# Performance work log

Hardware: AMD Instinct MI355X
Metric: run time of the kernel (lower is better)

## Reference

```python
import jax, jax.numpy as jnp
import numpy as np
import math

N, D, H = 4096, 2048, 16
HD = D // H  # head_dim = 128


def setup_inputs() -> dict:
    key = jax.random.key(0)
    ks = jax.random.split(key, 9)
    s = 1.0 / math.sqrt(D)
    return {
        "x":  jax.random.normal(ks[0], (N, D), dtype=jnp.float32),
        "Wq": jax.random.normal(ks[1], (D, D), dtype=jnp.float32) * s,
        "bq": jax.random.normal(ks[2], (D,), dtype=jnp.float32) * s,
        "Wk": jax.random.normal(ks[3], (D, D), dtype=jnp.float32) * s,
        "bk": jax.random.normal(ks[4], (D,), dtype=jnp.float32) * s,
        "Wv": jax.random.normal(ks[5], (D, D), dtype=jnp.float32) * s,
        "bv": jax.random.normal(ks[6], (D,), dtype=jnp.float32) * s,
        "Wo": jax.random.normal(ks[7], (D, D), dtype=jnp.float32) * s,
        "bo": jax.random.normal(ks[8], (D,), dtype=jnp.float32) * s,
    }


def reference(x, Wq, bq, Wk, bk, Wv, bv, Wo, bo):
    # eqx.nn.Linear: y = W @ x + b, weight shape (out, in) -> x @ W.T + b
    q = x @ Wq.T + bq            # [N, D]
    k = x @ Wk.T + bk            # [N, D]
    v = x @ Wv.T + bv            # [N, D]
    q = q.reshape(N, H, HD).transpose(1, 0, 2)   # [H, N, hd]
    k = k.reshape(N, H, HD).transpose(1, 2, 0)   # [H, hd, N]
    v = v.reshape(N, H, HD).transpose(1, 0, 2)   # [H, N, hd]
    scale = 1.0 / math.sqrt(HD)
    scores = jnp.matmul(q * scale, k)            # [H, N, N]
    attn = jax.nn.softmax(scores, axis=-1)
    ctx = jnp.matmul(attn, v)                    # [H, N, hd]
    ctx = ctx.transpose(1, 0, 2).reshape(N, D)   # [N, D]
    return ctx @ Wo.T + bo
```

## Files before the change

### kernel.cpp

```cpp
#include <hip/hip_runtime.h>
#include <stdint.h>

#define N_TOK 4096
#define DIM   2048
#define NH    16
#define HD    128
#define NW    (DIM * DIM)

using bf16x8 = __attribute__((ext_vector_type(8))) short;
using bf16x4 = __attribute__((ext_vector_type(4))) short;
using f32x4  = __attribute__((ext_vector_type(4))) float;

#if __has_builtin(__builtin_amdgcn_exp2f)
#define EXP2(x) __builtin_amdgcn_exp2f(x)
#else
#define EXP2(x) exp2f(x)
#endif

__device__ inline unsigned short f2bf(float f) {
  union { float f; unsigned u; } v; v.f = f;
  unsigned r = v.u + 0x7FFFu + ((v.u >> 16) & 1u);
  return (unsigned short)(r >> 16);
}
__device__ inline float bf2f(unsigned short u) {
  union { unsigned u; float f; } v; v.u = ((unsigned)u) << 16; return v.f;
}
__device__ inline f32x4 mfma16(bf16x8 a, bf16x8 b, f32x4 c) {
  return __builtin_amdgcn_mfma_f32_16x16x32_bf16(a, b, c, 0, 0, 0);
}
__device__ inline void gll16(const unsigned short* g, unsigned short* l) {
  __builtin_amdgcn_global_load_lds(
      (const __attribute__((address_space(1))) void*)g,
      (__attribute__((address_space(3))) void*)l, 16, 0, 0);
}

__global__ __launch_bounds__(256)
void cvt_bf16(const float* __restrict__ src, unsigned short* __restrict__ dst, int n) {
  int i = blockIdx.x * 256 + threadIdx.x;
  if (i * 8 >= n) return;
  const float4* s = (const float4*)src + (size_t)i * 2;
  float4 a = s[0], b = s[1];
  bf16x8 o;
  o[0] = (short)f2bf(a.x); o[1] = (short)f2bf(a.y);
  o[2] = (short)f2bf(a.z); o[3] = (short)f2bf(a.w);
  o[4] = (short)f2bf(b.x); o[5] = (short)f2bf(b.y);
  o[6] = (short)f2bf(b.z); o[7] = (short)f2bf(b.w);
  *(bf16x8*)(dst + (size_t)i * 8) = o;
}

template<int OUT_MODE>
__global__ __launch_bounds__(256)
void gemm_bf16(const unsigned short* __restrict__ A, const unsigned short* __restrict__ B,
               const float* __restrict__ bias, void* __restrict__ out_, float scale) {
  __shared__ unsigned short Asl[128 * 32];
  __shared__ unsigned short Bsl[128 * 32];
  const int tid  = threadIdx.x;
  const int lane = tid & 63, w = tid >> 6;
  const int wy = w >> 1, wx = w & 1;
  const int lr = lane & 15, quad = lane >> 4;
  const int m0 = blockIdx.y * 128, n0 = blockIdx.x * 128;

  const f32x4 vzero = {0.f, 0.f, 0.f, 0.f};
  f32x4 acc[4][4];
#pragma unroll
  for (int i = 0; i < 4; ++i)
#pragma unroll
    for (int j = 0; j < 4; ++j) acc[i][j] = vzero;

  for (int k0 = 0; k0 < DIM; k0 += 32) {
    __syncthreads();
#pragma unroll
    for (int i = 0; i < 2; ++i) {
      int ch = tid + i * 256;
      int r = ch >> 2, cc = ch & 3;
      gll16(&A[(size_t)(m0 + r) * DIM + k0 + cc * 8], &Asl[ch * 8]);
      gll16(&B[(size_t)(n0 + r) * DIM + k0 + cc * 8], &Bsl[ch * 8]);
    }
    __syncthreads();

    bf16x8 af[4], bfv[4];
#pragma unroll
    for (int mb = 0; mb < 4; ++mb)
      af[mb] = *(const bf16x8*)&Asl[(wy * 64 + mb * 16 + lr) * 32 + quad * 8];
#pragma unroll
    for (int nb = 0; nb < 4; ++nb)
      bfv[nb] = *(const bf16x8*)&Bsl[(wx * 64 + nb * 16 + lr) * 32 + quad * 8];
#pragma unroll
    for (int mb = 0; mb < 4; ++mb)
#pragma unroll
      for (int nb = 0; nb < 4; ++nb)
        acc[mb][nb] = mfma16(af[mb], bfv[nb], acc[mb][nb]);
  }

#pragma unroll
  for (int mb = 0; mb < 4; ++mb)
#pragma unroll
    for (int nb = 0; nb < 4; ++nb) {
      int gn = n0 + wx * 64 + nb * 16 + lr;
      int gm_base = m0 + wy * 64 + mb * 16 + quad * 4;
      float bs = bias[gn];
      if constexpr (OUT_MODE == 2) {
        bf16x4 pk;
#pragma unroll
        for (int r = 0; r < 4; ++r) pk[r] = (short)f2bf((acc[mb][nb][r] + bs) * scale);
        *(bf16x4*)&((unsigned short*)out_)[(size_t)gn * N_TOK + gm_base] = pk;
      } else {
#pragma unroll
        for (int r = 0; r < 4; ++r) {
          float v = (acc[mb][nb][r] + bs) * scale;
          if constexpr (OUT_MODE == 1)
            ((float*)out_)[(size_t)(gm_base + r) * DIM + gn] = v;
          else
            ((unsigned short*)out_)[(size_t)(gm_base + r) * DIM + gn] = f2bf(v);
        }
      }
    }
}

__global__ __launch_bounds__(256)
void flash_attn(const unsigned short* __restrict__ Q,
                const unsigned short* __restrict__ K,
                const unsigned short* __restrict__ Vt,
                unsigned short* __restrict__ ctx) {
  constexpr int LDK = 136;
  constexpr int LDV = 72;
  constexpr int LDP = 72;
  __shared__ unsigned short Ksl[64 * LDK];
  __shared__ unsigned short VTsl[128 * LDV];
  __shared__ unsigned short Psl[4][32 * LDP];

  const int tid  = threadIdx.x;
  const int lane = tid & 63, w = tid >> 6;
  const int lr = lane & 15, quad = lane >> 4;
  const int hoff = blockIdx.y * HD;
  const int q0   = blockIdx.x * 128;
  const int qw   = q0 + w * 32;

  bf16x8 qf[2][4];
#pragma unroll
  for (int mb = 0; mb < 2; ++mb)
#pragma unroll
    for (int c = 0; c < 4; ++c)
      qf[mb][c] = *(const bf16x8*)&Q[(size_t)(qw + mb * 16 + lr) * DIM + hoff + c * 32 + quad * 8];

  const f32x4 vzero = {0.f, 0.f, 0.f, 0.f};
  f32x4 o[2][8];
  float l_part[2][4];
#pragma unroll
  for (int mb = 0; mb < 2; ++mb) {
#pragma unroll
    for (int nb = 0; nb < 8; ++nb) o[mb][nb] = vzero;
#pragma unroll
    for (int r = 0; r < 4; ++r) l_part[mb][r] = 0.f;
  }

  bf16x8 kreg[4], vreg[4];
  auto load_tile = [&](int kt) {
    int kbase = kt * 64;
#pragma unroll
    for (int i = 0; i < 4; ++i) {
      int ch = tid + i * 256;
      kreg[i] = *(const bf16x8*)&K[(size_t)(kbase + (ch >> 4)) * DIM + hoff + (ch & 15) * 8];
      vreg[i] = *(const bf16x8*)&Vt[(size_t)(hoff + (ch >> 3)) * N_TOK + kbase + (ch & 7) * 8];
    }
  };
  load_tile(0);

  for (int kt = 0; kt < N_TOK / 64; ++kt) {
    __syncthreads();
#pragma unroll
    for (int i = 0; i < 4; ++i) {
      int ch = tid + i * 256;
      *(bf16x8*)&Ksl[(ch >> 4) * LDK + (ch & 15) * 8] = kreg[i];
      *(bf16x8*)&VTsl[(ch >> 3) * LDV + (ch & 7) * 8] = vreg[i];
    }
    __syncthreads();
    if (kt + 1 < N_TOK / 64) load_tile(kt + 1);

    f32x4 s[2][4];
#pragma unroll
    for (int mb = 0; mb < 2; ++mb)
#pragma unroll
      for (int nf = 0; nf < 4; ++nf) s[mb][nf] = vzero;
#pragma unroll
    for (int nf = 0; nf < 4; ++nf)
#pragma unroll
      for (int c = 0; c < 4; ++c) {
        bf16x8 kf = *(const bf16x8*)&Ksl[(nf * 16 + lr) * LDK + c * 32 + quad * 8];
#pragma unroll
        for (int mb = 0; mb < 2; ++mb) s[mb][nf] = mfma16(qf[mb][c], kf, s[mb][nf]);
      }

#pragma unroll
    for (int mb = 0; mb < 2; ++mb)
#pragma unroll
      for (int nf = 0; nf < 4; ++nf)
#pragma unroll
        for (int r = 0; r < 4; ++r) {
          unsigned short us = f2bf(EXP2(s[mb][nf][r]));
          l_part[mb][r] += bf2f(us);
          Psl[w][(mb * 16 + quad * 4 + r) * LDP + nf * 16 + lr] = us;
        }
    __asm__ volatile("s_waitcnt lgkmcnt(0)" ::: "memory");

    bf16x8 pf[2][2];
#pragma unroll
    for (int mb = 0; mb < 2; ++mb)
#pragma unroll
      for (int ki = 0; ki < 2; ++ki)
        pf[mb][ki] = *(const bf16x8*)&Psl[w][(mb * 16 + lr) * LDP + ki * 32 + quad * 8];

#pragma unroll
    for (int nb = 0; nb < 8; ++nb)
#pragma unroll
      for (int ki = 0; ki < 2; ++ki) {
        bf16x8 vf = *(const bf16x8*)&VTsl[(nb * 16 + lr) * LDV + ki * 32 + quad * 8];
#pragma unroll
        for (int mb = 0; mb < 2; ++mb) o[mb][nb] = mfma16(pf[mb][ki], vf, o[mb][nb]);
      }
  }

#pragma unroll
  for (int mb = 0; mb < 2; ++mb)
#pragma unroll
    for (int r = 0; r < 4; ++r) {
      float t = l_part[mb][r];
      t += __shfl_xor(t, 1);
      t += __shfl_xor(t, 2);
      t += __shfl_xor(t, 4);
      t += __shfl_xor(t, 8);
      float inv = 1.0f / t;
      int gq = qw + mb * 16 + quad * 4 + r;
#pragma unroll
      for (int nb = 0; nb < 8; ++nb)
        ctx[(size_t)gq * DIM + hoff + nb * 16 + lr] = f2bf(o[mb][nb][r] * inv);
    }
}

extern "C" void kernel_launch(void* const* d_in, const int* in_sizes, int n_in,
                              void* d_out, int out_size, void* d_ws, size_t ws_size,
                              hipStream_t stream) {
  (void)in_sizes; (void)n_in; (void)out_size; (void)ws_size;
  const float* x  = (const float*)d_in[0];
  const float* Wq = (const float*)d_in[1];
  const float* bq = (const float*)d_in[2];
  const float* Wk = (const float*)d_in[3];
  const float* bk = (const float*)d_in[4];
  const float* Wv = (const float*)d_in[5];
  const float* bv = (const float*)d_in[6];
  const float* Wo = (const float*)d_in[7];
  const float* bo = (const float*)d_in[8];

  const size_t NE = (size_t)N_TOK * DIM;
  unsigned short* xb  = (unsigned short*)d_ws;
  unsigned short* Wqb = xb + NE;
  unsigned short* Wkb = Wqb + NW;
  unsigned short* Wvb = Wkb + NW;
  unsigned short* Wob = Wvb + NW;
  unsigned short* Qb  = Wob + NW;
  unsigned short* Kb  = Qb + NE;
  unsigned short* Vtb = Kb + NE;

  cvt_bf16<<<4096, 256, 0, stream>>>(x,  xb,  (int)NE);
  cvt_bf16<<<2048, 256, 0, stream>>>(Wq, Wqb, NW);
  cvt_bf16<<<2048, 256, 0, stream>>>(Wk, Wkb, NW);
  cvt_bf16<<<2048, 256, 0, stream>>>(Wv, Wvb, NW);
  cvt_bf16<<<2048, 256, 0, stream>>>(Wo, Wob, NW);

  dim3 gemm_grid(DIM / 128, N_TOK / 128);
  const float qscale = 1.4426950408889634f * 0.08838834764831845f;

  gemm_bf16<0><<<gemm_grid, 256, 0, stream>>>(xb, Wqb, bq, Qb, qscale);
  gemm_bf16<0><<<gemm_grid, 256, 0, stream>>>(xb, Wkb, bk, Kb, 1.0f);
  gemm_bf16<2><<<gemm_grid, 256, 0, stream>>>(xb, Wvb, bv, Vtb, 1.0f);

  unsigned short* ctxb = xb;
  flash_attn<<<dim3(N_TOK / 128, NH), 256, 0, stream>>>(Qb, Kb, Vtb, ctxb);

  gemm_bf16<1><<<gemm_grid, 256, 0, stream>>>(ctxb, Wob, bo, (float*)d_out, 1.0f);
}
```

Measured before the change: 531.6 us.

## Merge conversion and QKV launches, shrink attention tile and reuse K LDS for P

Folds the five fp32-to-bf16 conversion launches into one kernel, and merges the three Q/K/V projection GEMMs into one launch with a 48-wide grid. Flash attention now gives each wave 16 query rows instead of 32, and 64 query rows per block. It packs P into bf16 pairs through lane shuffles and stores them in the K shared-memory region, with an extra barrier before doing so. The row sum now accumulates unrounded fp32 exp values. The aim is to cut launch overhead, raise occupancy (launch bounds 256,4, smaller LDS) and reduce LDS traffic, at the cost of reading K/V twice as often per query and one more sync per tile.

```diff
diff --git a/kernel.cpp b/kernel.cpp
--- a/kernel.cpp
+++ b/kernel.cpp
@@ -22,8 +22,9 @@
   unsigned r = v.u + 0x7FFFu + ((v.u >> 16) & 1u);
   return (unsigned short)(r >> 16);
 }
-__device__ inline float bf2f(unsigned short u) {
-  union { unsigned u; float f; } v; v.u = ((unsigned)u) << 16; return v.f;
+__device__ inline unsigned pack_bf16(float lo, float hi) {
+  union { float f; unsigned u; } a, b; a.f = lo; b.f = hi;
+  return ((b.u + 0x8000u) & 0xFFFF0000u) | ((a.u + 0x8000u) >> 16);
 }
 __device__ inline f32x4 mfma16(bf16x8 a, bf16x8 b, f32x4 c) {
   return __builtin_amdgcn_mfma_f32_16x16x32_bf16(a, b, c, 0, 0, 0);
@@ -35,23 +36,107 @@
 }
 
 __global__ __launch_bounds__(256)
-void cvt_bf16(const float* __restrict__ src, unsigned short* __restrict__ dst, int n) {
-  int i = blockIdx.x * 256 + threadIdx.x;
-  if (i * 8 >= n) return;
-  const float4* s = (const float4*)src + (size_t)i * 2;
-  float4 a = s[0], b = s[1];
+void cvt_all(const float* __restrict__ x, const float* __restrict__ wq,
+             const float* __restrict__ wk, const float* __restrict__ wv,
+             const float* __restrict__ wo,
+             unsigned short* __restrict__ xb, unsigned short* __restrict__ wqb,
+             unsigned short* __restrict__ wkb, unsigned short* __restrict__ wvb,
+             unsigned short* __restrict__ wob) {
+  int bid = blockIdx.x;
+  const float* s; unsigned short* d; int lb;
+  if (bid < 4096) { s = x; d = xb; lb = bid; }
+  else {
+    int t = (bid - 4096) >> 11, r = (bid - 4096) & 2047;
+    s = (t == 0) ? wq : (t == 1) ? wk : (t == 2) ? wv : wo;
+    d = (t == 0) ? wqb : (t == 1) ? wkb : (t == 2) ? wvb : wob;
+    lb = r;
+  }
+  size_t i = ((size_t)lb * 256 + threadIdx.x) * 8;
+  const float4* sp = (const float4*)(s + i);
+  float4 a = sp[0], b = sp[1];
   bf16x8 o;
   o[0] = (short)f2bf(a.x); o[1] = (short)f2bf(a.y);
   o[2] = (short)f2bf(a.z); o[3] = (short)f2bf(a.w);
   o[4] = (short)f2bf(b.x); o[5] = (short)f2bf(b.y);
   o[6] = (short)f2bf(b.z); o[7] = (short)f2bf(b.w);
-  *(bf16x8*)(dst + (size_t)i * 8) = o;
-}
-
-template<int OUT_MODE>
+  *(bf16x8*)(d + i) = o;
+}
+
 __global__ __launch_bounds__(256)
-void gemm_bf16(const unsigned short* __restrict__ A, const unsigned short* __restrict__ B,
-               const float* __restrict__ bias, void* __restrict__ out_, float scale) {
+void gemm_qkv(const unsigned short* __restrict__ A,
+              const unsigned short* __restrict__ Bq, const unsigned short* __restrict__ Bk,
+              const unsigned short* __restrict__ Bv,
+              const float* __restrict__ bq, const float* __restrict__ bk,
+              const float* __restrict__ bv,
+              unsigned short* __restrict__ Qb, unsigned short* __restrict__ Kb,
+              unsigned short* __restrict__ Vtb, float qscale) {
+  __shared__ unsigned short Asl[128 * 32];
+  __shared__ unsigned short Bsl[128 * 32];
+  const int wsel = blockIdx.x >> 4;
+  const unsigned short* B = (wsel == 0) ? Bq : (wsel == 1) ? Bk : Bv;
+  const float* bias = (wsel == 0) ? bq : (wsel == 1) ? bk : bv;
+  const float scale = (wsel == 0) ? qscale : 1.0f;
+  const int tid  = threadIdx.x;
+  const int lane = tid & 63, w = tid >> 6;
+  const int wy = w >> 1, wx = w & 1;
+  const int lr = lane & 15, quad = lane >> 4;
+  const int m0 = blockIdx.y * 128, n0 = (blockIdx.x & 15) * 128;
+
+  const f32x4 vzero = {0.f, 0.f, 0.f, 0.f};
+  f32x4 acc[4][4];
+#pragma unroll
+  for (int i = 0; i < 4; ++i)
+#pragma unroll
+    for (int j = 0; j < 4; ++j) acc[i][j] = vzero;
+
+  for (int k0 = 0; k0 < DIM; k0 += 32) {
+    __syncthreads();
+#pragma unroll
+    for (int i = 0; i < 2; ++i) {
+      int ch = tid + i * 256;
+      int r = ch >> 2, cc = ch & 3;
+      gll16(&A[(size_t)(m0 + r) * DIM + k0 + cc * 8], &Asl[ch * 8]);
+      gll16(&B[(size_t)(n0 + r) * DIM + k0 + cc * 8], &Bsl[ch * 8]);
+    }
+    __syncthreads();
+    bf16x8 af[4], bfv[4];
+#pragma unroll
+    for (int mb = 0; mb < 4; ++mb)
+      af[mb] = *(const bf16x8*)&Asl[(wy * 64 + mb * 16 + lr) * 32 + quad * 8];
+#pragma unroll
+    for (int nb = 0; nb < 4; ++nb)
+      bfv[nb] = *(const bf16x8*)&Bsl[(wx * 64 + nb * 16 + lr) * 32 + quad * 8];
+#pragma unroll
+    for (int mb = 0; mb < 4; ++mb)
+#pragma unroll
+      for (int nb = 0; nb < 4; ++nb)
+        acc[mb][nb] = mfma16(af[mb], bfv[nb], acc[mb][nb]);
+  }
+
+#pragma unroll
+  for (int mb = 0; mb < 4; ++mb)
+#pragma unroll
+    for (int nb = 0; nb < 4; ++nb) {
+      int gn = n0 + wx * 64 + nb * 16 + lr;
+      int gm_base = m0 + wy * 64 + mb * 16 + quad * 4;
+      float bs = bias[gn];
+      if (wsel == 2) {
+        bf16x4 pk;
+#pragma unroll
+        for (int r = 0; r < 4; ++r) pk[r] = (short)f2bf(acc[mb][nb][r] + bs);
+        *(bf16x4*)&Vtb[(size_t)gn * N_TOK + gm_base] = pk;
+      } else {
+        unsigned short* out = (wsel == 0) ? Qb : Kb;
+#pragma unroll
+        for (int r = 0; r < 4; ++r)
+          out[(size_t)(gm_base + r) * DIM + gn] = f2bf((acc[mb][nb][r] + bs) * scale);
+      }
+    }
+}
+
+__global__ __launch_bounds__(256)
+void gemm_out(const unsigned short* __restrict__ A, const unsigned short* __restrict__ B,
+              const float* __restrict__ bias, float* __restrict__ out) {
   __shared__ unsigned short Asl[128 * 32];
   __shared__ unsigned short Bsl[128 * 32];
   const int tid  = threadIdx.x;
@@ -77,7 +162,6 @@
       gll16(&B[(size_t)(n0 + r) * DIM + k0 + cc * 8], &Bsl[ch * 8]);
     }
     __syncthreads();
-
     bf16x8 af[4], bfv[4];
 #pragma unroll
     for (int mb = 0; mb < 4; ++mb)
@@ -99,60 +183,41 @@
       int gn = n0 + wx * 64 + nb * 16 + lr;
       int gm_base = m0 + wy * 64 + mb * 16 + quad * 4;
       float bs = bias[gn];
-      if constexpr (OUT_MODE == 2) {
-        bf16x4 pk;
-#pragma unroll
-        for (int r = 0; r < 4; ++r) pk[r] = (short)f2bf((acc[mb][nb][r] + bs) * scale);
-        *(bf16x4*)&((unsigned short*)out_)[(size_t)gn * N_TOK + gm_base] = pk;
-      } else {
-#pragma unroll
-        for (int r = 0; r < 4; ++r) {
-          float v = (acc[mb][nb][r] + bs) * scale;
-          if constexpr (OUT_MODE == 1)
-            ((float*)out_)[(size_t)(gm_base + r) * DIM + gn] = v;
-          else
-            ((unsigned short*)out_)[(size_t)(gm_base + r) * DIM + gn] = f2bf(v);
-        }
-      }
-    }
-}
-
-__global__ __launch_bounds__(256)
+#pragma unroll
+      for (int r = 0; r < 4; ++r)
+        out[(size_t)(gm_base + r) * DIM + gn] = acc[mb][nb][r] + bs;
+    }
+}
+
+__global__ __launch_bounds__(256, 4)
 void flash_attn(const unsigned short* __restrict__ Q,
                 const unsigned short* __restrict__ K,
                 const unsigned short* __restrict__ Vt,
                 unsigned short* __restrict__ ctx) {
-  constexpr int LDK = 136;
+  constexpr int LDK = 144;
   constexpr int LDV = 72;
   constexpr int LDP = 72;
   __shared__ unsigned short Ksl[64 * LDK];
   __shared__ unsigned short VTsl[128 * LDV];
-  __shared__ unsigned short Psl[4][32 * LDP];
 
   const int tid  = threadIdx.x;
   const int lane = tid & 63, w = tid >> 6;
   const int lr = lane & 15, quad = lane >> 4;
   const int hoff = blockIdx.y * HD;
-  const int q0   = blockIdx.x * 128;
-  const int qw   = q0 + w * 32;
-
-  bf16x8 qf[2][4];
-#pragma unroll
-  for (int mb = 0; mb < 2; ++mb)
-#pragma unroll
-    for (int c = 0; c < 4; ++c)
-      qf[mb][c] = *(const bf16x8*)&Q[(size_t)(qw + mb * 16 + lr) * DIM + hoff + c * 32 + quad * 8];
+  const int qw   = blockIdx.x * 64 + w * 16;
+  const bool odd = lane & 1;
+  unsigned short* Pw = Ksl + w * (16 * LDP);
+
+  bf16x8 qf[4];
+#pragma unroll
+  for (int c = 0; c < 4; ++c)
+    qf[c] = *(const bf16x8*)&Q[(size_t)(qw + lr) * DIM + hoff + c * 32 + quad * 8];
 
   const f32x4 vzero = {0.f, 0.f, 0.f, 0.f};
-  f32x4 o[2][8];
-  float l_part[2][4];
-#pragma unroll
-  for (int mb = 0; mb < 2; ++mb) {
-#pragma unroll
-    for (int nb = 0; nb < 8; ++nb) o[mb][nb] = vzero;
-#pragma unroll
-    for (int r = 0; r < 4; ++r) l_part[mb][r] = 0.f;
-  }
+  f32x4 o[8];
+  float l_part[4] = {0.f, 0.f, 0.f, 0.f};
+#pragma unroll
+  for (int nb = 0; nb < 8; ++nb) o[nb] = vzero;
 
   bf16x8 kreg[4], vreg[4];
   auto load_tile = [&](int kt) {
@@ -177,64 +242,68 @@
     __syncthreads();
     if (kt + 1 < N_TOK / 64) load_tile(kt + 1);
 
-    f32x4 s[2][4];
-#pragma unroll
-    for (int mb = 0; mb < 2; ++mb)
-#pragma unroll
-      for (int nf = 0; nf < 4; ++nf) s[mb][nf] = vzero;
+    f32x4 s[4];
+#pragma unroll
+    for (int nf = 0; nf < 4; ++nf) s[nf] = vzero;
 #pragma unroll
     for (int nf = 0; nf < 4; ++nf)
 #pragma unroll
       for (int c = 0; c < 4; ++c) {
         bf16x8 kf = *(const bf16x8*)&Ksl[(nf * 16 + lr) * LDK + c * 32 + quad * 8];
-#pragma unroll
-        for (int mb = 0; mb < 2; ++mb) s[mb][nf] = mfma16(qf[mb][c], kf, s[mb][nf]);
-      }
-
-#pragma unroll
-    for (int mb = 0; mb < 2; ++mb)
-#pragma unroll
-      for (int nf = 0; nf < 4; ++nf)
-#pragma unroll
-        for (int r = 0; r < 4; ++r) {
-          unsigned short us = f2bf(EXP2(s[mb][nf][r]));
-          l_part[mb][r] += bf2f(us);
-          Psl[w][(mb * 16 + quad * 4 + r) * LDP + nf * 16 + lr] = us;
-        }
+        s[nf] = mfma16(qf[c], kf, s[nf]);
+      }
+
+#pragma unroll
+    for (int nf = 0; nf < 4; ++nf)
+#pragma unroll
+      for (int r = 0; r < 4; ++r) {
+        float p = EXP2(s[nf][r]);
+        s[nf][r] = p;
+        l_part[r] += p;
+      }
+
+    __syncthreads();
+
+#pragma unroll
+    for (int pb = 0; pb < 2; ++pb)
+#pragma unroll
+      for (int r = 0; r < 4; ++r) {
+        float vA = s[2 * pb][r], vB = s[2 * pb + 1][r];
+        float oA = __shfl_xor(vA, 1), oB = __shfl_xor(vB, 1);
+        float lo = odd ? oB : vA;
+        float hi = odd ? vB : oA;
+        int nfS = 2 * pb + (int)odd;
+        *(unsigned*)&Pw[(quad * 4 + r) * LDP + nfS * 16 + (lr >> 1) * 2] = pack_bf16(lo, hi);
+      }
     __asm__ volatile("s_waitcnt lgkmcnt(0)" ::: "memory");
 
-    bf16x8 pf[2][2];
-#pragma unroll
-    for (int mb = 0; mb < 2; ++mb)
-#pragma unroll
-      for (int ki = 0; ki < 2; ++ki)
-        pf[mb][ki] = *(const bf16x8*)&Psl[w][(mb * 16 + lr) * LDP + ki * 32 + quad * 8];
+    bf16x8 pf[2];
+#pragma unroll
+    for (int ki = 0; ki < 2; ++ki)
+      pf[ki] = *(const bf16x8*)&Pw[lr * LDP + ki * 32 + quad * 8];
 
 #pragma unroll
     for (int nb = 0; nb < 8; ++nb)
 #pragma unroll
       for (int ki = 0; ki < 2; ++ki) {
         bf16x8 vf = *(const bf16x8*)&VTsl[(nb * 16 + lr) * LDV + ki * 32 + quad * 8];
-#pragma unroll
-        for (int mb = 0; mb < 2; ++mb) o[mb][nb] = mfma16(pf[mb][ki], vf, o[mb][nb]);
-      }
-  }
-
-#pragma unroll
-  for (int mb = 0; mb < 2; ++mb)
-#pragma unroll
-    for (int r = 0; r < 4; ++r) {
-      float t = l_part[mb][r];
-      t += __shfl_xor(t, 1);
-      t += __shfl_xor(t, 2);
-      t += __shfl_xor(t, 4);
-      t += __shfl_xor(t, 8);
-      float inv = 1.0f / t;
-      int gq = qw + mb * 16 + quad * 4 + r;
-#pragma unroll
-      for (int nb = 0; nb < 8; ++nb)
-        ctx[(size_t)gq * DIM + hoff + nb * 16 + lr] = f2bf(o[mb][nb][r] * inv);
-    }
+        o[nb] = mfma16(pf[ki], vf, o[nb]);
+      }
+  }
+
+#pragma unroll
+  for (int r = 0; r < 4; ++r) {
+    float t = l_part[r];
+    t += __shfl_xor(t, 1);
+    t += __shfl_xor(t, 2);
+    t += __shfl_xor(t, 4);
+    t += __shfl_xor(t, 8);
+    float inv = 1.0f / t;
+    int gq = qw + quad * 4 + r;
+#pragma unroll
+    for (int nb = 0; nb < 8; ++nb)
+      ctx[(size_t)gq * DIM + hoff + nb * 16 + lr] = f2bf(o[nb][r] * inv);
+  }
 }
 
 extern "C" void kernel_launch(void* const* d_in, const int* in_sizes, int n_in,
@@ -261,21 +330,14 @@
   unsigned short* Kb  = Qb + NE;
   unsigned short* Vtb = Kb + NE;
 
-  cvt_bf16<<<4096, 256, 0, stream>>>(x,  xb,  (int)NE);
-  cvt_bf16<<<2048, 256, 0, stream>>>(Wq, Wqb, NW);
-  cvt_bf16<<<2048, 256, 0, stream>>>(Wk, Wkb, NW);
-  cvt_bf16<<<2048, 256, 0, stream>>>(Wv, Wvb, NW);
-  cvt_bf16<<<2048, 256, 0, stream>>>(Wo, Wob, NW);
-
-  dim3 gemm_grid(DIM / 128, N_TOK / 128);
+  cvt_all<<<12288, 256, 0, stream>>>(x, Wq, Wk, Wv, Wo, xb, Wqb, Wkb, Wvb, Wob);
+
   const float qscale = 1.4426950408889634f * 0.08838834764831845f;
-
-  gemm_bf16<0><<<gemm_grid, 256, 0, stream>>>(xb, Wqb, bq, Qb, qscale);
-  gemm_bf16<0><<<gemm_grid, 256, 0, stream>>>(xb, Wkb, bk, Kb, 1.0f);
-  gemm_bf16<2><<<gemm_grid, 256, 0, stream>>>(xb, Wvb, bv, Vtb, 1.0f);
+  gemm_qkv<<<dim3(48, 32), 256, 0, stream>>>(xb, Wqb, Wkb, Wvb, bq, bk, bv,
+                                             Qb, Kb, Vtb, qscale);
 
   unsigned short* ctxb = xb;
-  flash_attn<<<dim3(N_TOK / 128, NH), 256, 0, stream>>>(Qb, Kb, Vtb, ctxb);
-
-  gemm_bf16<1><<<gemm_grid, 256, 0, stream>>>(ctxb, Wob, bo, (float*)d_out, 1.0f);
-}
+  flash_attn<<<dim3(N_TOK / 64, NH), 256, 0, stream>>>(Qb, Kb, Vtb, ctxb);
+
+  gemm_out<<<dim3(DIM / 128, N_TOK / 128), 256, 0, stream>>>(ctxb, Wob, bo, (float*)d_out);
+}
```

Result: slower. 585.9 us (+10.2%).
